# Kernel tuning notes

Hardware: AMD Instinct MI355X
Metric: run time of the kernel (lower is better)

## Reference

```python
import jax, jax.numpy as jnp
import numpy as np

N_SEGMENTS = 50
SEQ_LEN, BATCH, D_MODEL, N_HEADS = 6400, 2, 2048, 16


def setup_inputs() -> dict:
    key = jax.random.key(0)
    k1, k2, k3, k4 = jax.random.split(key, 4)
    scale = 1.0 / np.sqrt(D_MODEL)
    return {
        "hidden_states": jax.random.normal(k1, (SEQ_LEN, BATCH, D_MODEL), jnp.float32),
        "sequence_mask": jnp.ones((BATCH, SEQ_LEN), bool),
        "w_qkv": jax.random.normal(k2, (D_MODEL, 3 * D_MODEL), jnp.float32) * scale,
        "w_o": jax.random.normal(k3, (D_MODEL, D_MODEL), jnp.float32) * scale,
        "balance_factors": jax.random.normal(k4, (N_HEADS,), jnp.float32),
    }


def _local_attn(q, k, v, key_mask):
    # q,k,v: [B,H,S,Dh]; key_mask: [B,S] bool. Causal softmax attention within a segment.
    S, dh = q.shape[2], q.shape[3]
    scores = jnp.einsum('bhqd,bhkd->bhqk', q, k) / jnp.sqrt(jnp.asarray(dh, q.dtype))
    mask = jnp.tril(jnp.ones((S, S), bool))[None, None] & key_mask[:, None, None, :]
    scores = jnp.where(mask, scores, jnp.asarray(-1e9, q.dtype))
    p = jax.nn.softmax(scores, axis=-1)
    return jnp.einsum('bhqk,bhkd->bhqd', p, v)


def reference(hidden_states, sequence_mask, w_qkv, w_o, balance_factors):
    S, B, D = hidden_states.shape
    H = balance_factors.shape[0]
    dh = D // H
    seg = S // N_SEGMENTS

    x = hidden_states.reshape(N_SEGMENTS, seg, B, D)
    qkv = jnp.einsum('nsbd,de->nsbe', x, w_qkv).reshape(N_SEGMENTS, seg, B, 3, H, dh)
    # -> [N, B, H, seg, dh]
    q = jnp.transpose(qkv[:, :, :, 0], (0, 2, 3, 1, 4))
    k = jnp.transpose(qkv[:, :, :, 1], (0, 2, 3, 1, 4))
    v = jnp.transpose(qkv[:, :, :, 2], (0, 2, 3, 1, 4))

    mask_seg = jnp.transpose(sequence_mask.reshape(B, N_SEGMENTS, seg), (1, 0, 2))  # [N,B,seg]
    local_out = jax.vmap(_local_attn)(q, k, v, mask_seg)  # [N,B,H,seg,dh]

    # ELU+1 feature maps for the compressive memory (per InfiniAttention)
    sq = jax.nn.elu(q) + 1.0
    sk = jax.nn.elu(k) + 1.0

    # Segment 0: no memory yet -> retrieved is zeros; update without delta rule.
    mem0 = jnp.einsum('bhsd,bhse->bhde', sk[0], v[0])  # [B,H,dk,dv]
    norm0 = sk[0].sum(axis=2)                          # [B,H,dk]
    retrieved0 = jnp.zeros_like(local_out[0])

    def step(carry, xs):
        mem, norm = carry
        sq_n, sk_n, v_n = xs
        retr = jnp.einsum('bhsd,bhde->bhse', sq_n, mem)
        retr = retr / jnp.einsum('bhsd,bhd->bhs', sq_n, norm)[..., None]
        # delta rule: subtract what memory already predicts for these keys
        prev_v = jnp.einsum('bhsd,bhde->bhse', sk_n, mem)
        prev_v = prev_v / jnp.einsum('bhsd,bhd->bhs', sk_n, norm)[..., None]
        new_v = v_n - prev_v
        mem = mem + jnp.einsum('bhsd,bhse->bhde', sk_n, new_v)
        norm = norm + sk_n.sum(axis=2)
        return (mem, norm), retr

    (_, _), retrieved_rest = jax.lax.scan(step, (mem0, norm0), (sq[1:], sk[1:], v[1:]))
    retrieved = jnp.concatenate([retrieved0[None], retrieved_rest], axis=0)  # [N,B,H,seg,dh]

    g = jax.nn.sigmoid(balance_factors)[None, None, :, None, None]
    attn = g * retrieved + (1.0 - g) * local_out  # [N,B,H,seg,dh]
    attn = jnp.transpose(attn, (0, 3, 1, 2, 4)).reshape(S, B, D)  # [S,B,D]
    return jnp.einsum('sbd,de->sbe', attn, w_o)
```

## Files before the change

### kernel.cpp

```cpp
#include <hip/hip_runtime.h>
#include <hip/hip_bf16.h>

typedef __bf16 bf16;
typedef __bf16 bf16x8 __attribute__((ext_vector_type(8)));
typedef __bf16 bf16x4 __attribute__((ext_vector_type(4)));
typedef float  f32x4  __attribute__((ext_vector_type(4)));

#define S_LEN   6400
#define NBATCH  2
#define DMODEL  2048
#define NHEADS  16
#define DHEAD   128
#define NSEG    50
#define SEGLEN  128
#define MROWS   (S_LEN*NBATCH)
#define QKV_N   (3*DMODEL)

static __device__ __forceinline__ f32x4 mfma16x16x32(bf16x8 a, bf16x8 b, f32x4 c) {
    return __builtin_amdgcn_mfma_f32_16x16x32_bf16(a, b, c, 0, 0, 0);
}
static __device__ __forceinline__ void gload_lds16(const bf16* g, bf16* l) {
    __builtin_amdgcn_global_load_lds(
        (const __attribute__((address_space(1))) void*)g,
        (__attribute__((address_space(3))) void*)l, 16, 0, 0);
}
static __device__ __forceinline__ float elu1(float x) {
    return x > 0.f ? x + 1.f : __expf(x);
}

__global__ void prep_inputs(const float* __restrict__ hidden, bf16* __restrict__ abf,
                            const float* __restrict__ w_qkv, bf16* __restrict__ wqkvT,
                            const float* __restrict__ w_o,   bf16* __restrict__ woT)
{
    __shared__ float tile[32][33];
    const int bid = blockIdx.x;
    if (bid < 2048) {
        const int n8 = MROWS*DMODEL/8;
        const int stride = 2048 * 256;
        for (int i = bid * 256 + threadIdx.x; i < n8; i += stride) {
            const float4* p = (const float4*)(hidden + (size_t)i * 8);
            float4 v0 = p[0], v1 = p[1];
            bf16x8 o;
            o[0]=(bf16)v0.x; o[1]=(bf16)v0.y; o[2]=(bf16)v0.z; o[3]=(bf16)v0.w;
            o[4]=(bf16)v1.x; o[5]=(bf16)v1.y; o[6]=(bf16)v1.z; o[7]=(bf16)v1.w;
            *(bf16x8*)(abf + (size_t)i * 8) = o;
        }
        return;
    }
    const float* W; bf16* WT; int N, n0, k0;
    if (bid < 14336) {
        const int b2 = bid - 2048;
        W = w_qkv; WT = wqkvT; N = QKV_N;
        n0 = (b2 % 192) * 32; k0 = (b2 / 192) * 32;
    } else {
        const int b3 = bid - 14336;
        W = w_o; WT = woT; N = DMODEL;
        n0 = (b3 % 64) * 32; k0 = (b3 / 64) * 32;
    }
    const int tx = threadIdx.x & 31, ty = threadIdx.x >> 5;
    #pragma unroll
    for (int i = 0; i < 4; i++) {
        int kk = ty + i * 8;
        tile[kk][tx] = W[(size_t)(k0 + kk) * N + n0 + tx];
    }
    __syncthreads();
    #pragma unroll
    for (int i = 0; i < 4; i++) {
        int nn = ty + i * 8;
        WT[(size_t)(n0 + nn) * DMODEL + k0 + tx] = (bf16)tile[tx][nn];
    }
}

template<bool CBF16>
__global__ __launch_bounds__(512, 2) void gemm256(const bf16* __restrict__ A,
                                                  const bf16* __restrict__ BT,
                                                  void* __restrict__ Cptr, int Ndim)
{
    constexpr int K = DMODEL;
    constexpr int NT = K / 32;
    __shared__ __align__(16) bf16 a_sm[2][256*32];
    __shared__ __align__(16) bf16 b_sm[2][256*32];

    const int tid = threadIdx.x;
    const int l = tid & 63, wid = tid >> 6;
    const int wm = wid >> 2, wn = wid & 3;
    const int brow = blockIdx.x * 256, bcol = blockIdx.y * 256;
    const int l15 = l & 15, lg = l >> 4;

    const int st_mr  = tid >> 3;
    const int st_s0  = (tid & 7) ^ (st_mr & 7);
    const int st_row = 2 * st_mr + (st_s0 >> 2);
    const int st_col = (st_s0 & 3) << 3;
    const bf16* Asrc = A  + (size_t)(brow + st_row) * K + st_col;
    const bf16* Bsrc = BT + (size_t)(bcol + st_row) * K + st_col;

    int aoff[8], boff[4];
    #pragma unroll
    for (int mi = 0; mi < 8; mi++) {
        const int r = wm*128 + mi*16 + l15, mr = r >> 1;
        aoff[mi] = mr*64 + ((((( r & 1) << 2) | lg) ^ (mr & 7)) << 3);
    }
    #pragma unroll
    for (int ni = 0; ni < 4; ni++) {
        const int r = wn*64 + ni*16 + l15, mr = r >> 1;
        boff[ni] = mr*64 + ((((( r & 1) << 2) | lg) ^ (mr & 7)) << 3);
    }

    f32x4 acc[8][4];
    #pragma unroll
    for (int mi = 0; mi < 8; mi++)
        #pragma unroll
        for (int ni = 0; ni < 4; ni++)
            #pragma unroll
            for (int e = 0; e < 4; e++) acc[mi][ni][e] = 0.f;

    auto STAGE = [&](int buf, int kt2) {
        const int k0 = kt2 * 32;
        #pragma unroll
        for (int i = 0; i < 2; i++) {
            gload_lds16(Asrc + (size_t)(i*128) * K + k0, &a_sm[buf][i*4096 + tid*8]);
            gload_lds16(Bsrc + (size_t)(i*128) * K + k0, &b_sm[buf][i*4096 + tid*8]);
        }
    };

    bf16x8 af[4], ag[4], bfr[4];
    auto READ0 = [&](int buf) {
        #pragma unroll
        for (int mi = 0; mi < 4; mi++) af[mi]  = *(const bf16x8*)&a_sm[buf][aoff[mi]];
        #pragma unroll
        for (int ni = 0; ni < 4; ni++) bfr[ni] = *(const bf16x8*)&b_sm[buf][boff[ni]];
    };
    auto READ1 = [&](int buf) {
        #pragma unroll
        for (int mi = 0; mi < 4; mi++) ag[mi] = *(const bf16x8*)&a_sm[buf][aoff[4 + mi]];
    };
    auto MFMA_LO = [&]() {
        __builtin_amdgcn_s_setprio(1);
        #pragma unroll
        for (int mi = 0; mi < 4; mi++)
            #pragma unroll
            for (int ni = 0; ni < 4; ni++)
                acc[mi][ni] = mfma16x16x32(af[mi], bfr[ni], acc[mi][ni]);
        __builtin_amdgcn_s_setprio(0);
    };
    auto MFMA_HI = [&]() {
        __builtin_amdgcn_s_setprio(1);
        #pragma unroll
        for (int mi = 0; mi < 4; mi++)
            #pragma unroll
            for (int ni = 0; ni < 4; ni++)
                acc[4 + mi][ni] = mfma16x16x32(ag[mi], bfr[ni], acc[4 + mi][ni]);
        __builtin_amdgcn_s_setprio(0);
    };

    STAGE(0, 0);
    STAGE(1, 1);
    asm volatile("s_waitcnt vmcnt(4)" ::: "memory");
    __builtin_amdgcn_sched_barrier(0);
    __builtin_amdgcn_s_barrier();
    READ0(0);

    for (int tp = 0; tp < NT - 2; tp += 2) {
        READ1(0);
        __builtin_amdgcn_sched_barrier(0);
        MFMA_LO();
        asm volatile("s_waitcnt lgkmcnt(0)" ::: "memory");
        __builtin_amdgcn_sched_barrier(0);
        __builtin_amdgcn_s_barrier();
        STAGE(0, tp + 2);
        __builtin_amdgcn_sched_barrier(0);
        MFMA_HI();
        asm volatile("s_waitcnt vmcnt(4)" ::: "memory");
        __builtin_amdgcn_sched_barrier(0);
        __builtin_amdgcn_s_barrier();

        READ0(1);
        READ1(1);
        __builtin_amdgcn_sched_barrier(0);
        MFMA_LO();
        asm volatile("s_waitcnt lgkmcnt(0)" ::: "memory");
        __builtin_amdgcn_sched_barrier(0);
        __builtin_amdgcn_s_barrier();
        STAGE(1, tp + 3);
        __builtin_amdgcn_sched_barrier(0);
        MFMA_HI();
        asm volatile("s_waitcnt vmcnt(4)" ::: "memory");
        __builtin_amdgcn_sched_barrier(0);
        __builtin_amdgcn_s_barrier();
        READ0(0);
    }

    READ1(0);
    __builtin_amdgcn_sched_barrier(0);
    MFMA_LO();
    asm volatile("s_waitcnt lgkmcnt(0)" ::: "memory");
    __builtin_amdgcn_sched_barrier(0);
    MFMA_HI();
    asm volatile("s_waitcnt vmcnt(0)" ::: "memory");
    __builtin_amdgcn_sched_barrier(0);
    __builtin_amdgcn_s_barrier();
    READ0(1);
    READ1(1);
    __builtin_amdgcn_sched_barrier(0);
    MFMA_LO();
    asm volatile("s_waitcnt lgkmcnt(0)" ::: "memory");
    __builtin_amdgcn_sched_barrier(0);
    MFMA_HI();

    #pragma unroll
    for (int mi = 0; mi < 8; mi++)
        #pragma unroll
        for (int ni = 0; ni < 4; ni++) {
            const int row = brow + wm*128 + mi*16 + lg*4;
            const int col = bcol + wn*64 + ni*16 + l15;
            #pragma unroll
            for (int j = 0; j < 4; j++) {
                float v = acc[mi][ni][j];
                if (CBF16) ((bf16*)Cptr)[(size_t)(row + j) * Ndim + col] = (bf16)v;
                else       ((float*)Cptr)[(size_t)(row + j) * Ndim + col] = v;
            }
        }
}

__global__ void attn_local(const bf16* __restrict__ qkv,
                           bf16* __restrict__ lob,
                           const float* __restrict__ bal,
                           float* __restrict__ ksum)
{
    __shared__ bf16 qp_sm[128*136];
    __shared__ bf16 k_sm [128*136];
    __shared__ bf16 vT_sm[128*136];
    const int bid = blockIdx.x;
    const int h = bid & 15, b = (bid >> 4) & 1, n = bid >> 5;
    const int tid = threadIdx.x, l = tid & 63, w = tid >> 6;
    const int l15 = l & 15, lk = (l >> 4) * 8, r0 = (l >> 4) * 4;
    const float g  = 1.f / (1.f + __expf(-bal[h]));
    const float w1 = 1.f - g;

    {
        const int srow = tid >> 1, off = (tid & 1) << 6;
        const size_t gb = ((size_t)(n*SEGLEN + srow)*NBATCH + b)*QKV_N + h*DHEAD + off;
        const bf16* qsrc = qkv + gb;
        const bf16* ksrc = qkv + gb + DMODEL;
        const bf16* vsrc = qkv + gb + 2*DMODEL;
        #pragma unroll
        for (int j = 0; j < 64; j += 8) {
            *(bf16x8*)&qp_sm[srow*136 + off + j] = *(const bf16x8*)(qsrc + j);
            *(bf16x8*)&k_sm [srow*136 + off + j] = *(const bf16x8*)(ksrc + j);
        }
        #pragma unroll
        for (int j = 0; j < 64; j++) vT_sm[(off + j)*136 + srow] = vsrc[j];
    }
    __syncthreads();

    f32x4 sc[2][8];
    for (int mi = 0; mi < 2; mi++) for (int ni = 0; ni < 8; ni++)
        for (int e = 0; e < 4; e++) sc[mi][ni][e] = 0.f;
    #pragma unroll
    for (int ks = 0; ks < 4; ks++) {
        const int ko = ks*32 + lk;
        bf16x8 aq[2], bk[8];
        #pragma unroll
        for (int mi = 0; mi < 2; mi++)
            aq[mi] = *(const bf16x8*)&qp_sm[(w*32 + mi*16 + l15)*136 + ko];
        #pragma unroll
        for (int ni = 0; ni < 8; ni++)
            bk[ni] = *(const bf16x8*)&k_sm[(ni*16 + l15)*136 + ko];
        #pragma unroll
        for (int mi = 0; mi < 2; mi++)
            #pragma unroll
            for (int ni = 0; ni < 8; ni++)
                sc[mi][ni] = mfma16x16x32(aq[mi], bk[ni], sc[mi][ni]);
    }
    __syncthreads();

    const float scale = 0.088388347648318433f;
    #pragma unroll
    for (int mi = 0; mi < 2; mi++) {
        #pragma unroll
        for (int j = 0; j < 4; j++) {
            const int R = w*32 + mi*16 + r0 + j;
            float v[8]; float mx = -1e30f;
            #pragma unroll
            for (int ni = 0; ni < 8; ni++) {
                float x = sc[mi][ni][j] * scale;
                if (ni*16 + l15 > R) x = -1e9f;
                v[ni] = x; mx = fmaxf(mx, x);
            }
            #pragma unroll
            for (int d = 1; d < 16; d <<= 1) mx = fmaxf(mx, __shfl_xor(mx, d));
            float sum = 0.f;
            #pragma unroll
            for (int ni = 0; ni < 8; ni++) { v[ni] = __expf(v[ni] - mx); sum += v[ni]; }
            #pragma unroll
            for (int d = 1; d < 16; d <<= 1) sum += __shfl_xor(sum, d);
            const float inv = 1.f / sum;
            #pragma unroll
            for (int ni = 0; ni < 8; ni++)
                qp_sm[R*136 + ni*16 + l15] = (bf16)(v[ni] * inv);
        }
    }
    __syncthreads();

    f32x4 o[2][8];
    for (int mi = 0; mi < 2; mi++) for (int ni = 0; ni < 8; ni++)
        for (int e = 0; e < 4; e++) o[mi][ni][e] = 0.f;
    #pragma unroll
    for (int ks = 0; ks < 4; ks++) {
        const int ko = ks*32 + lk;
        bf16x8 ap[2], bv[8];
        #pragma unroll
        for (int mi = 0; mi < 2; mi++)
            ap[mi] = *(const bf16x8*)&qp_sm[(w*32 + mi*16 + l15)*136 + ko];
        #pragma unroll
        for (int ni = 0; ni < 8; ni++)
            bv[ni] = *(const bf16x8*)&vT_sm[(ni*16 + l15)*136 + ko];
        #pragma unroll
        for (int mi = 0; mi < 2; mi++)
            #pragma unroll
            for (int ni = 0; ni < 8; ni++)
                o[mi][ni] = mfma16x16x32(ap[mi], bv[ni], o[mi][ni]);
    }

    #pragma unroll
    for (int mi = 0; mi < 2; mi++)
        #pragma unroll
        for (int ni = 0; ni < 8; ni++) {
            const int R = w*32 + mi*16 + r0;
            const int c = ni*16 + l15;
            #pragma unroll
            for (int j = 0; j < 4; j++)
                lob[((size_t)(n*SEGLEN + R + j)*NBATCH + b)*DMODEL + h*DHEAD + c] =
                    (bf16)(w1 * o[mi][ni][j]);
        }

    if (tid < 128) {
        float a = 0.f;
        for (int ss = 0; ss < 128; ss++) a += elu1((float)k_sm[ss*136 + tid]);
        ksum[((size_t)(b*NHEADS + h)*NSEG + n)*128 + tid] = a;
    }
}

__global__ void prefix_norm(const float* __restrict__ ksum, float* __restrict__ normprev)
{
    const int bh = blockIdx.x, dk = threadIdx.x;
    float a = 0.f;
    for (int n = 0; n < NSEG; n++) {
        const size_t i = ((size_t)bh*NSEG + n)*128 + dk;
        normprev[i] = a;
        a += ksum[i];
    }
}

__global__ __launch_bounds__(256) void prep_U(const bf16* __restrict__ qkv,
                                              const float* __restrict__ normprev,
                                              bf16* __restrict__ Ub,
                                              float* __restrict__ denqb,
                                              float* __restrict__ invkb)
{
    __shared__ bf16  skT[128*136];
    __shared__ bf16  vT [128*136];
    __shared__ float norm_sm[128];
    __shared__ float partq[256], partk[256];

    const int n = blockIdx.x, bh = blockIdx.y;
    const int b = bh >> 4, h = bh & 15;
    const size_t seg = (size_t)bh*NSEG + n;
    const int tid = threadIdx.x, l = tid & 63, w = tid >> 6;
    const int wr = w >> 1, wc = w & 1;
    const int l15 = l & 15, lk = (l >> 4) * 8, r0 = (l >> 4) * 4;
    const int s = tid >> 1, off = (tid & 1) << 6;

    const size_t rowb = ((size_t)(n*SEGLEN + s)*NBATCH + b)*QKV_N + h*DHEAD + off;
    {
        #pragma unroll
        for (int j = 0; j < 64; j += 8) {
            bf16x8 kv = *(const bf16x8*)(qkv + rowb + DMODEL + j);
            bf16x8 vv = *(const bf16x8*)(qkv + rowb + 2*DMODEL + j);
            #pragma unroll
            for (int e = 0; e < 8; e++) {
                skT[(off + j + e)*136 + s] = (bf16)elu1((float)kv[e]);
                vT [(off + j + e)*136 + s] = vv[e];
            }
        }
    }
    if (tid < 128) norm_sm[tid] = (n > 0) ? normprev[seg*128 + tid] : 0.f;
    __syncthreads();

    if (n > 0) {
        float aq = 0.f;
        #pragma unroll
        for (int j = 0; j < 64; j += 8) {
            bf16x8 qa = *(const bf16x8*)(qkv + rowb + j);
            #pragma unroll
            for (int e = 0; e < 8; e++) aq += elu1((float)qa[e]) * norm_sm[off + j + e];
        }
        float ak = 0.f;
        for (int d = off; d < off + 64; d++) ak += (float)skT[d*136 + s] * norm_sm[d];
        partq[tid] = aq; partk[tid] = ak;
    }
    __syncthreads();
    if (n > 0 && tid < 128) {
        denqb[seg*128 + tid] = partq[tid*2] + partq[tid*2 + 1];
        invkb[seg*128 + tid] = 1.f / (partk[tid*2] + partk[tid*2 + 1]);
    }

    f32x4 ua[4][4];
    for (int mi = 0; mi < 4; mi++) for (int ni = 0; ni < 4; ni++)
        for (int e = 0; e < 4; e++) ua[mi][ni][e] = 0.f;
    #pragma unroll
    for (int ks = 0; ks < 4; ks++) {
        const int ko = ks*32 + lk;
        bf16x8 af[4], bv[4];
        #pragma unroll
        for (int mi = 0; mi < 4; mi++)
            af[mi] = *(const bf16x8*)&skT[(wr*64 + mi*16 + l15)*136 + ko];
        #pragma unroll
        for (int ni = 0; ni < 4; ni++)
            bv[ni] = *(const bf16x8*)&vT[(wc*64 + ni*16 + l15)*136 + ko];
        #pragma unroll
        for (int mi = 0; mi < 4; mi++)
            #pragma unroll
            for (int ni = 0; ni < 4; ni++)
                ua[mi][ni] = mfma16x16x32(af[mi], bv[ni], ua[mi][ni]);
    }
    #pragma unroll
    for (int mi = 0; mi < 4; mi++)
        #pragma unroll
        for (int ni = 0; ni < 4; ni++) {
            const int row = wr*64 + mi*16 + r0, col = wc*64 + ni*16 + l15;
            #pragma unroll
            for (int j = 0; j < 4; j++)
                Ub[(seg << 14) + (size_t)(row + j)*128 + col] = (bf16)ua[mi][ni][j];
        }
}

__global__ __launch_bounds__(256, 1) void scan2(const bf16* __restrict__ qkv,
                                                const bf16* __restrict__ Ub,
                                                const float* __restrict__ denqb,
                                                const float* __restrict__ invkb,
                                                bf16* __restrict__ lob,
                                                const float* __restrict__ bal)
{
    __shared__ bf16 memT[16*136];
    __shared__ bf16 skT [128*136];
    __shared__ bf16 yT  [16*136];
    const int bid = blockIdx.x;
    const int bh = bid & 31, dq = bid >> 5;
    const int b = bh >> 4, h = bh & 15;
    const int tid = threadIdx.x, l = tid & 63, w = tid >> 6;
    const int l15 = l & 15, lk = (l >> 4) * 8, r0 = (l >> 4) * 4;
    const float g = 1.f / (1.f + __expf(-bal[h]));
    const size_t segb = (size_t)bh * NSEG;
    const int cdv = dq*16 + l15;

    float mast[2][4];
    #pragma unroll
    for (int mi = 0; mi < 2; mi++)
        #pragma unroll
        for (int j = 0; j < 4; j++) {
            const int row = w*32 + mi*16 + r0 + j;
            mast[mi][j] = (float)Ub[(segb << 14) + (size_t)row*128 + cdv];
            memT[l15*136 + row] = (bf16)mast[mi][j];
        }
    __syncthreads();

    bf16x8 qA[8], kA[8], qB[8], kB[8];

    auto loadraw = [&](int n2, bf16x8* qr, bf16x8* kr) {
        #pragma unroll
        for (int mi = 0; mi < 2; mi++)
            #pragma unroll
            for (int ks = 0; ks < 4; ks++) {
                const size_t base =
                    ((size_t)(n2*SEGLEN + w*32 + mi*16 + l15)*NBATCH + b)*QKV_N
                    + h*DHEAD + ks*32 + lk;
                qr[mi*4 + ks] = *(const bf16x8*)(qkv + base);
                kr[mi*4 + ks] = *(const bf16x8*)(qkv + base + DMODEL);
            }
    };

    auto step = [&](int n, bf16x8* curq, bf16x8* curk, bf16x8* nxtq, bf16x8* nxtk) {
        float uval[2][4], lv[2][4], dqv[2][4], ivk[2][4];
        #pragma unroll
        for (int mi = 0; mi < 2; mi++)
            #pragma unroll
            for (int j = 0; j < 4; j++) {
                const int sx = w*32 + mi*16 + r0 + j;
                dqv[mi][j] = denqb[(segb + n)*128 + sx];
                ivk[mi][j] = invkb[(segb + n)*128 + sx];
                uval[mi][j] = (float)Ub[((segb + n) << 14) + (size_t)sx*128 + cdv];
                lv[mi][j] = (float)lob[((size_t)(n*SEGLEN + sx)*NBATCH + b)*DMODEL
                                       + h*DHEAD + cdv];
            }
        bf16x8 sqf[8], skf[8];
        #pragma unroll
        for (int f = 0; f < 8; f++) {
            bf16x8 qv = curq[f], kv = curk[f], sq_, sk_;
            #pragma unroll
            for (int e = 0; e < 8; e++) {
                sq_[e] = (bf16)elu1((float)qv[e]);
                sk_[e] = (bf16)elu1((float)kv[e]);
            }
            sqf[f] = sq_; skf[f] = sk_;
        }
        #pragma unroll
        for (int mi = 0; mi < 2; mi++)
            #pragma unroll
            for (int ks = 0; ks < 4; ks++)
                #pragma unroll
                for (int e = 0; e < 8; e++)
                    skT[(ks*32 + lk + e)*136 + w*32 + mi*16 + l15] = skf[mi*4 + ks][e];
        f32x4 racc[2], yacc[2];
        #pragma unroll
        for (int mi = 0; mi < 2; mi++)
            #pragma unroll
            for (int e = 0; e < 4; e++) { racc[mi][e] = 0.f; yacc[mi][e] = 0.f; }
        #pragma unroll
        for (int ks = 0; ks < 4; ks++) {
            bf16x8 bm = *(const bf16x8*)&memT[l15*136 + ks*32 + lk];
            #pragma unroll
            for (int mi = 0; mi < 2; mi++) {
                racc[mi] = mfma16x16x32(sqf[mi*4 + ks], bm, racc[mi]);
                yacc[mi] = mfma16x16x32(skf[mi*4 + ks], bm, yacc[mi]);
            }
        }
        if (n < NSEG - 1) loadraw(n + 1, nxtq, nxtk);
        #pragma unroll
        for (int mi = 0; mi < 2; mi++)
            #pragma unroll
            for (int j = 0; j < 4; j++)
                yT[l15*136 + w*32 + mi*16 + r0 + j] = (bf16)(yacc[mi][j] * ivk[mi][j]);
        __syncthreads();
        f32x4 zacc[2];
        #pragma unroll
        for (int mi = 0; mi < 2; mi++)
            #pragma unroll
            for (int e = 0; e < 4; e++) zacc[mi][e] = 0.f;
        #pragma unroll
        for (int ks = 0; ks < 4; ks++) {
            bf16x8 bz = *(const bf16x8*)&yT[l15*136 + ks*32 + lk];
            #pragma unroll
            for (int mi = 0; mi < 2; mi++) {
                bf16x8 az = *(const bf16x8*)&skT[(w*32 + mi*16 + l15)*136 + ks*32 + lk];
                zacc[mi] = mfma16x16x32(az, bz, zacc[mi]);
            }
        }
        #pragma unroll
        for (int mi = 0; mi < 2; mi++)
            #pragma unroll
            for (int j = 0; j < 4; j++) {
                const int sx = w*32 + mi*16 + r0 + j;
                const float rv = racc[mi][j] / dqv[mi][j];
                lob[((size_t)(n*SEGLEN + sx)*NBATCH + b)*DMODEL + h*DHEAD + cdv] =
                    (bf16)(lv[mi][j] + g * rv);
                mast[mi][j] += uval[mi][j] - zacc[mi][j];
                memT[l15*136 + sx] = (bf16)mast[mi][j];
            }
        __syncthreads();
    };

    loadraw(1, qA, kA);
    for (int n = 1; n < NSEG; n += 2) {
        step(n, qA, kA, qB, kB);
        if (n + 1 < NSEG) step(n + 1, qB, kB, qA, kA);
    }
}

extern "C" void kernel_launch(void* const* d_in, const int* in_sizes, int n_in,
                              void* d_out, int out_size, void* d_ws, size_t ws_size,
                              hipStream_t stream)
{
    (void)in_sizes; (void)n_in; (void)out_size; (void)ws_size;
    const float* hidden = (const float*)d_in[0];
    const float* w_qkv  = (const float*)d_in[2];
    const float* w_o    = (const float*)d_in[3];
    const float* bal    = (const float*)d_in[4];

    char* ws = (char*)d_ws;
    bf16*  qkvb  = (bf16*)ws;
    bf16*  lob   = (bf16*)(ws + 157286400);
    bf16*  woT   = (bf16*)(ws + 209715200);
    bf16*  abf   = (bf16*)(ws + 218103808);
    bf16*  Ub    = abf;
    bf16*  wqkvT = (bf16*)(ws + 270532608);
    float* ksum  = (float*)(ws + 270532608);
    float* normp = (float*)(ws + 271351808);
    float* denqb = (float*)(ws + 272171008);
    float* invkb = (float*)(ws + 272990208);

    dim3 blk(256);
    prep_inputs<<<18432, blk, 0, stream>>>(hidden, abf, w_qkv, wqkvT, w_o, woT);

    gemm256<true><<<dim3(MROWS/256, QKV_N/256), 512, 0, stream>>>(abf, wqkvT, qkvb, QKV_N);

    attn_local<<<dim3(NSEG*NBATCH*NHEADS), blk, 0, stream>>>(qkvb, lob, bal, ksum);
    prefix_norm<<<32, 128, 0, stream>>>(ksum, normp);
    prep_U<<<dim3(NSEG, 32), blk, 0, stream>>>(qkvb, normp, Ub, denqb, invkb);
    scan2<<<256, blk, 0, stream>>>(qkvb, Ub, denqb, invkb, lob, bal);

    gemm256<false><<<dim3(MROWS/256, DMODEL/256), 512, 0, stream>>>(lob, woT, d_out, DMODEL);
}
```

Measured before the change: 873.9 us.

## Fuse prep_U into attn_local and compute denominators inside scan

The sk^T·V product (U) is now computed in attn_local, which already loads K and V for each segment. This removes the separate prep_U kernel and its second read of K/V from global memory. The per-row normalization dot products (sq·norm and sk·norm) are now computed inside scan2 from the prefix norms using wave shuffles, instead of being precomputed and stored. In exchange, attn_local uses more LDS (a fourth 128x136 tile, which may lower occupancy) and the serial scan does extra ALU work on each step.

Result: no change. 865.5 us (-1.0%).

```diff
diff --git a/kernel.cpp b/kernel.cpp
--- a/kernel.cpp
+++ b/kernel.cpp
@@ -225,13 +225,16 @@
 __global__ void attn_local(const bf16* __restrict__ qkv,
                            bf16* __restrict__ lob,
                            const float* __restrict__ bal,
-                           float* __restrict__ ksum)
+                           float* __restrict__ ksum,
+                           bf16* __restrict__ Ub)
 {
-    __shared__ bf16 qp_sm[128*136];
-    __shared__ bf16 k_sm [128*136];
-    __shared__ bf16 vT_sm[128*136];
+    __shared__ bf16 qp_sm [128*136];
+    __shared__ bf16 k_sm  [128*136];
+    __shared__ bf16 vT_sm [128*136];
+    __shared__ bf16 skT_sm[128*136];
     const int bid = blockIdx.x;
     const int h = bid & 15, b = (bid >> 4) & 1, n = bid >> 5;
+    const int bh = b*NHEADS + h;
     const int tid = threadIdx.x, l = tid & 63, w = tid >> 6;
     const int l15 = l & 15, lk = (l >> 4) * 8, r0 = (l >> 4) * 4;
     const float g  = 1.f / (1.f + __expf(-bal[h]));
@@ -245,11 +248,16 @@
         const bf16* vsrc = qkv + gb + 2*DMODEL;
         #pragma unroll
         for (int j = 0; j < 64; j += 8) {
+            bf16x8 kv = *(const bf16x8*)(ksrc + j);
+            bf16x8 vv = *(const bf16x8*)(vsrc + j);
             *(bf16x8*)&qp_sm[srow*136 + off + j] = *(const bf16x8*)(qsrc + j);
-            *(bf16x8*)&k_sm [srow*136 + off + j] = *(const bf16x8*)(ksrc + j);
-        }
-        #pragma unroll
-        for (int j = 0; j < 64; j++) vT_sm[(off + j)*136 + srow] = vsrc[j];
+            *(bf16x8*)&k_sm [srow*136 + off + j] = kv;
+            #pragma unroll
+            for (int e = 0; e < 8; e++) {
+                vT_sm [(off + j + e)*136 + srow] = vv[e];
+                skT_sm[(off + j + e)*136 + srow] = (bf16)elu1((float)kv[e]);
+            }
+        }
     }
     __syncthreads();
 
@@ -336,8 +344,41 @@
 
     if (tid < 128) {
         float a = 0.f;
-        for (int ss = 0; ss < 128; ss++) a += elu1((float)k_sm[ss*136 + tid]);
-        ksum[((size_t)(b*NHEADS + h)*NSEG + n)*128 + tid] = a;
+        for (int ss = 0; ss < 128; ss++) a += (float)skT_sm[tid*136 + ss];
+        ksum[((size_t)bh*NSEG + n)*128 + tid] = a;
+    }
+
+    {
+        const int wr = w >> 1, wc = w & 1;
+        const size_t seg = (size_t)bh*NSEG + n;
+        f32x4 ua[4][4];
+        for (int mi = 0; mi < 4; mi++) for (int ni = 0; ni < 4; ni++)
+            for (int e = 0; e < 4; e++) ua[mi][ni][e] = 0.f;
+        #pragma unroll
+        for (int ks = 0; ks < 4; ks++) {
+            const int ko = ks*32 + lk;
+            bf16x8 auf[4], bv[4];
+            #pragma unroll
+            for (int mi = 0; mi < 4; mi++)
+                auf[mi] = *(const bf16x8*)&skT_sm[(wr*64 + mi*16 + l15)*136 + ko];
+            #pragma unroll
+            for (int ni = 0; ni < 4; ni++)
+                bv[ni] = *(const bf16x8*)&vT_sm[(wc*64 + ni*16 + l15)*136 + ko];
+            #pragma unroll
+            for (int mi = 0; mi < 4; mi++)
+                #pragma unroll
+                for (int ni = 0; ni < 4; ni++)
+                    ua[mi][ni] = mfma16x16x32(auf[mi], bv[ni], ua[mi][ni]);
+        }
+        #pragma unroll
+        for (int mi = 0; mi < 4; mi++)
+            #pragma unroll
+            for (int ni = 0; ni < 4; ni++) {
+                const int row = wr*64 + mi*16 + r0, col = wc*64 + ni*16 + l15;
+                #pragma unroll
+                for (int j = 0; j < 4; j++)
+                    Ub[(seg << 14) + (size_t)(row + j)*128 + col] = (bf16)ua[mi][ni][j];
+            }
     }
 }
 
@@ -352,93 +393,9 @@
     }
 }
 
-__global__ __launch_bounds__(256) void prep_U(const bf16* __restrict__ qkv,
-                                              const float* __restrict__ normprev,
-                                              bf16* __restrict__ Ub,
-                                              float* __restrict__ denqb,
-                                              float* __restrict__ invkb)
-{
-    __shared__ bf16  skT[128*136];
-    __shared__ bf16  vT [128*136];
-    __shared__ float norm_sm[128];
-    __shared__ float partq[256], partk[256];
-
-    const int n = blockIdx.x, bh = blockIdx.y;
-    const int b = bh >> 4, h = bh & 15;
-    const size_t seg = (size_t)bh*NSEG + n;
-    const int tid = threadIdx.x, l = tid & 63, w = tid >> 6;
-    const int wr = w >> 1, wc = w & 1;
-    const int l15 = l & 15, lk = (l >> 4) * 8, r0 = (l >> 4) * 4;
-    const int s = tid >> 1, off = (tid & 1) << 6;
-
-    const size_t rowb = ((size_t)(n*SEGLEN + s)*NBATCH + b)*QKV_N + h*DHEAD + off;
-    {
-        #pragma unroll
-        for (int j = 0; j < 64; j += 8) {
-            bf16x8 kv = *(const bf16x8*)(qkv + rowb + DMODEL + j);
-            bf16x8 vv = *(const bf16x8*)(qkv + rowb + 2*DMODEL + j);
-            #pragma unroll
-            for (int e = 0; e < 8; e++) {
-                skT[(off + j + e)*136 + s] = (bf16)elu1((float)kv[e]);
-                vT [(off + j + e)*136 + s] = vv[e];
-            }
-        }
-    }
-    if (tid < 128) norm_sm[tid] = (n > 0) ? normprev[seg*128 + tid] : 0.f;
-    __syncthreads();
-
-    if (n > 0) {
-        float aq = 0.f;
-        #pragma unroll
-        for (int j = 0; j < 64; j += 8) {
-            bf16x8 qa = *(const bf16x8*)(qkv + rowb + j);
-            #pragma unroll
-            for (int e = 0; e < 8; e++) aq += elu1((float)qa[e]) * norm_sm[off + j + e];
-        }
-        float ak = 0.f;
-        for (int d = off; d < off + 64; d++) ak += (float)skT[d*136 + s] * norm_sm[d];
-        partq[tid] = aq; partk[tid] = ak;
-    }
-    __syncthreads();
-    if (n > 0 && tid < 128) {
-        denqb[seg*128 + tid] = partq[tid*2] + partq[tid*2 + 1];
-        invkb[seg*128 + tid] = 1.f / (partk[tid*2] + partk[tid*2 + 1]);
-    }
-
-    f32x4 ua[4][4];
-    for (int mi = 0; mi < 4; mi++) for (int ni = 0; ni < 4; ni++)
-        for (int e = 0; e < 4; e++) ua[mi][ni][e] = 0.f;
-    #pragma unroll
-    for (int ks = 0; ks < 4; ks++) {
-        const int ko = ks*32 + lk;
-        bf16x8 af[4], bv[4];
-        #pragma unroll
-        for (int mi = 0; mi < 4; mi++)
-            af[mi] = *(const bf16x8*)&skT[(wr*64 + mi*16 + l15)*136 + ko];
-        #pragma unroll
-        for (int ni = 0; ni < 4; ni++)
-            bv[ni] = *(const bf16x8*)&vT[(wc*64 + ni*16 + l15)*136 + ko];
-        #pragma unroll
-        for (int mi = 0; mi < 4; mi++)
-            #pragma unroll
-            for (int ni = 0; ni < 4; ni++)
-                ua[mi][ni] = mfma16x16x32(af[mi], bv[ni], ua[mi][ni]);
-    }
-    #pragma unroll
-    for (int mi = 0; mi < 4; mi++)
-        #pragma unroll
-        for (int ni = 0; ni < 4; ni++) {
-            const int row = wr*64 + mi*16 + r0, col = wc*64 + ni*16 + l15;
-            #pragma unroll
-            for (int j = 0; j < 4; j++)
-                Ub[(seg << 14) + (size_t)(row + j)*128 + col] = (bf16)ua[mi][ni][j];
-        }
-}
-
 __global__ __launch_bounds__(256, 1) void scan2(const bf16* __restrict__ qkv,
                                                 const bf16* __restrict__ Ub,
-                                                const float* __restrict__ denqb,
-                                                const float* __restrict__ invkb,
+                                                const float* __restrict__ normp,
                                                 bf16* __restrict__ lob,
                                                 const float* __restrict__ bal)
 {
@@ -481,14 +438,12 @@
     };
 
     auto step = [&](int n, bf16x8* curq, bf16x8* curk, bf16x8* nxtq, bf16x8* nxtk) {
-        float uval[2][4], lv[2][4], dqv[2][4], ivk[2][4];
+        float uval[2][4], lv[2][4];
         #pragma unroll
         for (int mi = 0; mi < 2; mi++)
             #pragma unroll
             for (int j = 0; j < 4; j++) {
                 const int sx = w*32 + mi*16 + r0 + j;
-                dqv[mi][j] = denqb[(segb + n)*128 + sx];
-                ivk[mi][j] = invkb[(segb + n)*128 + sx];
                 uval[mi][j] = (float)Ub[((segb + n) << 14) + (size_t)sx*128 + cdv];
                 lv[mi][j] = (float)lob[((size_t)(n*SEGLEN + sx)*NBATCH + b)*DMODEL
                                        + h*DHEAD + cdv];
@@ -503,6 +458,36 @@
                 sk_[e] = (bf16)elu1((float)kv[e]);
             }
             sqf[f] = sq_; skf[f] = sk_;
+        }
+        float nrm[4][8];
+        {
+            const float* np = normp + (segb + n)*128;
+            #pragma unroll
+            for (int ks = 0; ks < 4; ks++) {
+                float4 a0 = *(const float4*)(np + ks*32 + lk);
+                float4 a1 = *(const float4*)(np + ks*32 + lk + 4);
+                nrm[ks][0]=a0.x; nrm[ks][1]=a0.y; nrm[ks][2]=a0.z; nrm[ks][3]=a0.w;
+                nrm[ks][4]=a1.x; nrm[ks][5]=a1.y; nrm[ks][6]=a1.z; nrm[ks][7]=a1.w;
+            }
+        }
+        float dqv[2][4], ivk[2][4];
+        #pragma unroll
+        for (int mi = 0; mi < 2; mi++) {
+            float aq = 0.f, ak = 0.f;
+            #pragma unroll
+            for (int ks = 0; ks < 4; ks++)
+                #pragma unroll
+                for (int e = 0; e < 8; e++) {
+                    aq += (float)sqf[mi*4 + ks][e] * nrm[ks][e];
+                    ak += (float)skf[mi*4 + ks][e] * nrm[ks][e];
+                }
+            aq += __shfl_xor(aq, 16); aq += __shfl_xor(aq, 32);
+            ak += __shfl_xor(ak, 16); ak += __shfl_xor(ak, 32);
+            #pragma unroll
+            for (int j = 0; j < 4; j++) {
+                dqv[mi][j] = __shfl(aq, r0 + j);
+                ivk[mi][j] = 1.f / __shfl(ak, r0 + j);
+            }
         }
         #pragma unroll
         for (int mi = 0; mi < 2; mi++)
@@ -586,18 +571,15 @@
     bf16*  wqkvT = (bf16*)(ws + 270532608);
     float* ksum  = (float*)(ws + 270532608);
     float* normp = (float*)(ws + 271351808);
-    float* denqb = (float*)(ws + 272171008);
-    float* invkb = (float*)(ws + 272990208);
 
     dim3 blk(256);
     prep_inputs<<<18432, blk, 0, stream>>>(hidden, abf, w_qkv, wqkvT, w_o, woT);
 
     gemm256<true><<<dim3(MROWS/256, QKV_N/256), 512, 0, stream>>>(abf, wqkvT, qkvb, QKV_N);
 
-    attn_local<<<dim3(NSEG*NBATCH*NHEADS), blk, 0, stream>>>(qkvb, lob, bal, ksum);
+    attn_local<<<dim3(NSEG*NBATCH*NHEADS), blk, 0, stream>>>(qkvb, lob, bal, ksum, Ub);
     prefix_norm<<<32, 128, 0, stream>>>(ksum, normp);
-    prep_U<<<dim3(NSEG, 32), blk, 0, stream>>>(qkvb, normp, Ub, denqb, invkb);
-    scan2<<<256, blk, 0, stream>>>(qkvb, Ub, denqb, invkb, lob, bal);
+    scan2<<<256, blk, 0, stream>>>(qkvb, Ub, normp, lob, bal);
 
     gemm256<false><<<dim3(MROWS/256, DMODEL/256), 512, 0, stream>>>(lob, woT, d_out, DMODEL);
 }
```
